# Performance work log

Hardware: AMD Instinct MI355X
Metric: run time of the kernel (lower is better)

## Reference

```python
import jax, jax.numpy as jnp
import numpy as np

B, H_, W_ = 8, 64, 64
N = H_ * W_
IN_DIM = 256
DIM = 256
HEADS = 8
DIM_HEAD = DIM // HEADS      # 32
DH2 = DIM_HEAD // 2          # 16
KC = 3                       # kernel_conv
WS = 8                       # window size
EPS = 1e-5


def _conv2d(x, w, b, groups):
    # x: [B, C, H, W], w: [O, C//groups, kh, kw], 'same' padding, stride 1
    y = jax.lax.conv_general_dilated(
        x, w, window_strides=(1, 1), padding=((1, 1), (1, 1)),
        dimension_numbers=('NCHW', 'OIHW', 'NCHW'), feature_group_count=groups)
    return y + b[None, :, None, None]


def _cross_shaped_attention(q, k, v, H, W, ws, horizontal,
                            fc_w, dep_w, dep_b, rate1, rate2):
    # q, k, v: [B, N, C] with C = dim/2 = 128; H*W == N (no padding path)
    Bq, Nq, C = q.shape
    nh = C // DIM_HEAD  # heads per half = 4
    # ---- parallel conv-attention branch ----
    # [B, 3*heads, dim_head//2, N]
    f = jnp.concatenate([t.reshape(Bq, HEADS, DH2, Nq) for t in (q, k, v)], axis=1)
    # 1x1 conv fc: (heads*3=24) -> (kc*kc=9) channels
    f_all = jnp.einsum('oc,bcst->bost', fc_w, f)           # [B, 9, 16, N]
    f_conv = jnp.transpose(f_all, (0, 2, 1, 3)).reshape(Bq, DH2 * KC * KC, H, W)  # [B,144,H,W]
    out_conv = _conv2d(f_conv, dep_w, dep_b, groups=DH2)   # [B, 128, H, W]
    out_conv = jnp.transpose(out_conv, (0, 2, 3, 1)).reshape(Bq, Nq, C)
    # ---- cross-shaped windowed attention ----
    scale = DIM_HEAD ** -0.5
    if horizontal:
        # window over rows: groups of ws full-width rows -> tokens ws*W
        def win(t):
            t = t.reshape(Bq, H // ws, ws, W, nh, DIM_HEAD)
            return jnp.transpose(t, (0, 1, 4, 2, 3, 5)).reshape(Bq, H // ws, nh, ws * W, DIM_HEAD)
    else:
        # window over cols: groups of ws full-height cols -> tokens ws*H
        def win(t):
            t = t.reshape(Bq, H, W // ws, ws, nh, DIM_HEAD)
            return jnp.transpose(t, (0, 2, 4, 3, 1, 5)).reshape(Bq, W // ws, nh, ws * H, DIM_HEAD)
    qw, kw, vw = win(q), win(k), win(v)
    attn = jnp.einsum('bgnqd,bgnkd->bgnqk', qw, kw) * scale  # [B, G, nh, L, L]
    attn = jax.nn.softmax(attn, axis=-1)
    o = jnp.einsum('bgnqk,bgnkd->bgnqd', attn, vw)           # [B, G, nh, L, dh]
    if horizontal:
        o = o.reshape(Bq, H // ws, nh, ws, W, DIM_HEAD)
        o = jnp.transpose(o, (0, 1, 3, 4, 2, 5)).reshape(Bq, Nq, C)  # B (Hg ws) W (nh dh)
    else:
        o = o.reshape(Bq, W // ws, nh, ws, H, DIM_HEAD)
        o = jnp.transpose(o, (0, 4, 1, 3, 2, 5)).reshape(Bq, Nq, C)  # B H (Wg ws) (nh dh)
    return rate1 * o + rate2 * out_conv


def reference(x, w_qkv, b_qkv, w_out, b_out, bn_g, bn_b, pconv_w, pconv_b,
              fc_w, dep_w, dep_b, rate1, rate2, H, W):
    Bx = x.shape[0]
    Nx = H * W
    qv = x @ w_qkv + b_qkv                       # [B, N, 2*dim]
    q, v = jnp.split(qv, 2, axis=-1)
    # parallel depthwise conv branch on v (hardswish -> dw 3x3)
    v_img = jnp.transpose(v.reshape(Bx, H, W, DIM), (0, 3, 1, 2))
    v_conv = _conv2d(jax.nn.hard_swish(v_img), pconv_w, pconv_b, groups=DIM)
    v_conv = jnp.transpose(v_conv.reshape(Bx, DIM, Nx), (0, 2, 1))   # [B, N, dim]
    qh, qv2 = jnp.split(q, 2, axis=-1)
    vh, vv = jnp.split(v, 2, axis=-1)
    # H % ws == 0 and W % ws == 0 -> no padding, no masks
    attn_h = _cross_shaped_attention(qh, vh, vh, H, W, WS, True,
                                     fc_w, dep_w, dep_b, rate1, rate2)
    attn_v = _cross_shaped_attention(qv2, vv, vv, H, W, WS, False,
                                     fc_w, dep_w, dep_b, rate1, rate2)
    a = jnp.concatenate([attn_h, attn_v], axis=-1) + v_conv
    a = jax.nn.hard_swish(a)
    a = a @ w_out + b_out
    # BatchNorm1d in training mode over flattened (B*N, dim), biased variance
    flat = a.reshape(Bx * Nx, DIM)
    mu = flat.mean(axis=0)
    var = flat.var(axis=0)
    flat = (flat - mu) * jax.lax.rsqrt(var + EPS) * bn_g + bn_b
    return flat.reshape(Bx, Nx, DIM)


def setup_inputs() -> dict:
    key = jax.random.key(0)
    ks = jax.random.split(key, 16)
    s = 0.02
    return {
        'x': jax.random.normal(ks[0], (B, N, IN_DIM), jnp.float32),
        'w_qkv': jax.random.normal(ks[1], (IN_DIM, 2 * DIM), jnp.float32) * s,
        'b_qkv': jax.random.normal(ks[2], (2 * DIM,), jnp.float32) * s,
        'w_out': jax.random.normal(ks[3], (DIM, DIM), jnp.float32) * s,
        'b_out': jax.random.normal(ks[4], (DIM,), jnp.float32) * s,
        'bn_g': jax.random.uniform(ks[5], (DIM,), jnp.float32, 0.5, 1.5),
        'bn_b': jax.random.normal(ks[6], (DIM,), jnp.float32) * s,
        'pconv_w': jax.random.normal(ks[7], (DIM, 1, 3, 3), jnp.float32) * s,
        'pconv_b': jax.random.normal(ks[8], (DIM,), jnp.float32) * s,
        'fc_w': jax.random.normal(ks[9], (KC * KC, HEADS * 3), jnp.float32) * s,
        'dep_w': jax.random.normal(ks[10], (IN_DIM // 2, KC * KC, 3, 3), jnp.float32) * s,
        'dep_b': jax.random.normal(ks[11], (IN_DIM // 2,), jnp.float32) * s,
        'rate1': jax.random.uniform(ks[12], (), jnp.float32, 0.4, 0.6),
        'rate2': jax.random.uniform(ks[13], (), jnp.float32, 0.4, 0.6),
        'H': H_,
        'W': W_,
    }
```

## Files before the change

kernel.cpp:

```cpp
#include <hip/hip_runtime.h>
#include <hip/hip_bf16.h>
#include <math.h>

constexpr int Bn   = 8;
constexpr int Hh   = 64;
constexpr int Ww   = 64;
constexpr int Nn   = Hh * Ww;
constexpr int Mrows = Bn * Nn;
constexpr int QKVC = 512;
constexpr int DIMc = 256;

typedef short short8 __attribute__((ext_vector_type(8)));
typedef float f32x16 __attribute__((ext_vector_type(16)));
typedef float f32x4 __attribute__((ext_vector_type(4)));

__device__ __forceinline__ float hswish(float x) {
    float r = fminf(fmaxf(x + 3.f, 0.f), 6.f);
    return x * r * (1.f / 6.f);
}

__device__ __forceinline__ ushort bf16u(float f) {
    return __bfloat16_as_ushort(__float2bfloat16(f));
}

__device__ __forceinline__ uint32_t pkbf(float a, float b) {
    return (uint32_t)bf16u(a) | ((uint32_t)bf16u(b) << 16);
}

__device__ __forceinline__ float dot2bf(uint32_t a, uint32_t b, float c) {
    asm("v_dot2_f32_bf16 %0, %1, %2, %0" : "+v"(c) : "v"(a), "v"(b));
    return c;
}

__device__ __forceinline__ float bflo(uint32_t p) {
    union { uint32_t u; float f; } c; c.u = p << 16; return c.f;
}
__device__ __forceinline__ float bfhi(uint32_t p) {
    union { uint32_t u; float f; } c; c.u = p & 0xFFFF0000u; return c.f;
}

#if __has_builtin(__builtin_amdgcn_permlane32_swap)
typedef int int2v __attribute__((ext_vector_type(2)));
__device__ __forceinline__ void plswap(uint32_t& a, uint32_t& b) {
    int2v r = __builtin_amdgcn_permlane32_swap((int)a, (int)b, false, false);
    a = (uint32_t)r.x; b = (uint32_t)r.y;
}
#else
__device__ __forceinline__ void plswap(uint32_t& a, uint32_t& b) {
    int l = threadIdx.x & 63;
    uint32_t sa = (uint32_t)__shfl_xor((int)a, 32);
    uint32_t sb = (uint32_t)__shfl_xor((int)b, 32);
    uint32_t na = (l < 32) ? a : sb;
    uint32_t nb = (l < 32) ? sa : b;
    a = na; b = nb;
}
#endif

__device__ __forceinline__ void gload_lds16(const ushort* g, ushort* l) {
    __builtin_amdgcn_global_load_lds(
        (const __attribute__((address_space(1))) unsigned int*)g,
        (__attribute__((address_space(3))) unsigned int*)l, 16, 0, 0);
}

__global__ __launch_bounds__(256) void cvtbf_kernel(
    const float* __restrict__ in, ushort* __restrict__ out)
{
    int i = (blockIdx.x * 256 + threadIdx.x) * 8;
    float4 f0 = *reinterpret_cast<const float4*>(&in[i]);
    float4 f1 = *reinterpret_cast<const float4*>(&in[i + 4]);
    float v[8] = {f0.x, f0.y, f0.z, f0.w, f1.x, f1.y, f1.z, f1.w};
    ushort o[8];
    #pragma unroll
    for (int j = 0; j < 8; ++j) o[j] = bf16u(v[j]);
    *reinterpret_cast<short8*>(&out[i]) = *reinterpret_cast<short8*>(o);
}

__global__ __launch_bounds__(256) void wtconv_kernel(
    const float* __restrict__ Wf, ushort* __restrict__ Wt, int K, int N)
{
    int idx = blockIdx.x * 256 + threadIdx.x;
    int n = idx / K, k = idx - n * K;
    Wt[idx] = bf16u(Wf[(size_t)k * N + n]);
}

__global__ __launch_bounds__(256) void weff_kernel(
    const float* __restrict__ dw, const float* __restrict__ fcw,
    uint32_t* __restrict__ Wp)
{
    int idx = blockIdx.x * 256 + threadIdx.x;
    if (idx >= 9216) return;
    int k = idx % 9;
    int a = (idx / 9) & 7;
    int oc = (idx / 72) & 7;
    int gi = idx / 576;
    float q = 0.f, v = 0.f;
    const float* dwp = &dw[(gi * 8 + oc) * 81 + k];
    #pragma unroll
    for (int ic = 0; ic < 9; ++ic) {
        float d = dwp[ic * 9];
        q += d * fcw[ic * 24 + a];
        v += d * (fcw[ic * 24 + 8 + a] + fcw[ic * 24 + 16 + a]);
    }
    Wp[idx] = pkbf(q, v);
}

template<bool OBF, bool STATS>
__global__ __launch_bounds__(256) void hgemm_kernel(
    const ushort* __restrict__ A, const ushort* __restrict__ Bt,
    const float* __restrict__ bias, void* __restrict__ Cv,
    float* __restrict__ stats, int M, int N, int K)
{
    __shared__ ushort As[128 * 32];
    __shared__ ushort Bs[128 * 32];
    const int tid = threadIdx.x;
    const int w = tid >> 6, l = tid & 63;
    const int brow = blockIdx.y * 128;
    const int bcol = blockIdx.x * 128;
    const int wm = (w >> 1) * 64, wn = (w & 1) * 64;

    f32x4 acc[4][4] = {};

    const int c0 = tid, c1 = tid + 256;
    const int r0 = c0 >> 2, q0 = (c0 & 3) ^ (r0 & 3);
    const int r1 = c1 >> 2, q1 = (c1 & 3) ^ (r1 & 3);
    const ushort* a0p = &A[(size_t)(brow + r0) * K + q0 * 8];
    const ushort* a1p = &A[(size_t)(brow + r1) * K + q1 * 8];
    const ushort* b0p = &Bt[(size_t)(bcol + r0) * K + q0 * 8];
    const ushort* b1p = &Bt[(size_t)(bcol + r1) * K + q1 * 8];
    ushort* asw0 = &As[(w * 64) * 8];
    ushort* asw1 = &As[(256 + w * 64) * 8];
    ushort* bsw0 = &Bs[(w * 64) * 8];
    ushort* bsw1 = &Bs[(256 + w * 64) * 8];

    const int fr = l & 15;
    const int qq = ((l >> 4) ^ (l & 3)) * 8;

    for (int k0 = 0; k0 < K; k0 += 32) {
        gload_lds16(a0p + k0, asw0);
        gload_lds16(a1p + k0, asw1);
        gload_lds16(b0p + k0, bsw0);
        gload_lds16(b1p + k0, bsw1);
        __syncthreads();
        short8 af[4], bf[4];
        #pragma unroll
        for (int i = 0; i < 4; ++i) {
            af[i] = *reinterpret_cast<const short8*>(&As[(wm + i * 16 + fr) * 32 + qq]);
            bf[i] = *reinterpret_cast<const short8*>(&Bs[(wn + i * 16 + fr) * 32 + qq]);
        }
        #pragma unroll
        for (int mi = 0; mi < 4; ++mi)
            #pragma unroll
            for (int ni = 0; ni < 4; ++ni)
                acc[mi][ni] = __builtin_amdgcn_mfma_f32_16x16x32_bf16(
                    af[mi], bf[ni], acc[mi][ni], 0, 0, 0);
        __syncthreads();
    }

    const int cr = l >> 4;
    #pragma unroll
    for (int ni = 0; ni < 4; ++ni) {
        int n = bcol + wn + ni * 16 + fr;
        float bv = bias[n];
        float s1 = 0.f, s2 = 0.f;
        #pragma unroll
        for (int mi = 0; mi < 4; ++mi) {
            int m = brow + wm + mi * 16 + cr * 4;
            #pragma unroll
            for (int r = 0; r < 4; ++r) {
                float val = acc[mi][ni][r] + bv;
                if (OBF)
                    ((ushort*)Cv)[(size_t)(m + r) * N + n] = bf16u(val);
                else
                    ((float*)Cv)[(size_t)(m + r) * N + n] = val;
                if (STATS) { s1 += val; s2 += val * val; }
            }
        }
        if (STATS) {
            s1 += __shfl_xor(s1, 16); s2 += __shfl_xor(s2, 16);
            s1 += __shfl_xor(s1, 32); s2 += __shfl_xor(s2, 32);
            if (cr == 0) {
                atomicAdd(&stats[n], s1);
                atomicAdd(&stats[256 + n], s2);
            }
        }
    }
}

__global__ __launch_bounds__(256) void vconv_kernel(
    const ushort* __restrict__ qvb, const float* __restrict__ pw,
    const float* __restrict__ pb, float* __restrict__ Abuf)
{
    int idx = blockIdx.x * 256 + threadIdx.x;
    int c2 = idx & 127;
    int n = (idx >> 7) & (Nn - 1);
    int b = idx >> 19;
    int x = n & 63, y = n >> 6;
    int ch = c2 * 2;
    float s0 = pb[ch], s1 = pb[ch + 1];
    float w0[9], w1[9];
    #pragma unroll
    for (int k = 0; k < 9; ++k) { w0[k] = pw[ch * 9 + k]; w1[k] = pw[ch * 9 + 9 + k]; }
    #pragma unroll
    for (int ky = 0; ky < 3; ++ky) {
        int yy = y + ky - 1;
        if (yy >= 0 && yy < Hh) {
            #pragma unroll
            for (int kx = 0; kx < 3; ++kx) {
                int xx = x + kx - 1;
                if (xx >= 0 && xx < Ww) {
                    uint32_t pk = *reinterpret_cast<const uint32_t*>(
                        &qvb[(size_t)(b * Nn + yy * Ww + xx) * QKVC + 256 + ch]);
                    s0 += hswish(bflo(pk)) * w0[ky * 3 + kx];
                    s1 += hswish(bfhi(pk)) * w1[ky * 3 + kx];
                }
            }
        }
    }
    float2 o; o.x = s0; o.y = s1;
    *reinterpret_cast<float2*>(&Abuf[(size_t)(b * Nn + n) * DIMc + ch]) = o;
}

__global__ __launch_bounds__(256) void convbranch_kernel(
    const ushort* __restrict__ qvb, const uint32_t* __restrict__ Wp,
    const float* __restrict__ db, const float* __restrict__ rate2p,
    float* __restrict__ Abuf)
{
    int blk = blockIdx.x;
    int ytile = blk & 3;
    int gi = (blk >> 2) & 15;
    int b = (blk >> 6) & 7;
    int branch = blk >> 9;
    int y0 = ytile * 16;
    int qoff = branch * 128;
    int coff = branch * 128;

    __shared__ uint32_t sqv[8][18][66];
    __shared__ uint32_t wpk[8][8][9];
    const int tid = threadIdx.x;

    for (int i = tid; i < 8 * 18 * 66; i += 256) {
        int xp = i % 66;
        int t2 = i / 66;
        int rr = t2 % 18;
        int a = t2 / 18;
        int x = xp - 1;
        int y = y0 + rr - 1;
        uint32_t pk = 0;
        if ((unsigned)x < 64u && (unsigned)y < 64u) {
            int token = (a * 16 + gi) * 32 + (y >> 1);
            int chan = (y & 1) * 64 + x;
            const ushort* p = &qvb[(size_t)(b * Nn + token) * QKVC + qoff + chan];
            pk = (uint32_t)p[0] | ((uint32_t)p[256] << 16);
        }
        sqv[a][rr][xp] = pk;
    }
    for (int i = tid; i < 576; i += 256)
        ((uint32_t*)wpk)[i] = Wp[gi * 576 + i];
    __syncthreads();

    const int x = tid & 63;
    const int w = tid >> 6;
    const int rh = (w & 1) * 8;
    const int oc0 = (w >> 1) * 4;

    float acc[4][8] = {};
    #pragma unroll 1
    for (int a = 0; a < 8; ++a) {
        uint32_t ipk[10][3];
        #pragma unroll
        for (int rr = 0; rr < 10; ++rr) {
            const uint32_t* rp = &sqv[a][rh + rr][x];
            ipk[rr][0] = rp[0]; ipk[rr][1] = rp[1]; ipk[rr][2] = rp[2];
        }
        #pragma unroll
        for (int ocl = 0; ocl < 4; ++ocl) {
            #pragma unroll
            for (int ky = 0; ky < 3; ++ky)
                #pragma unroll
                for (int kx = 0; kx < 3; ++kx) {
                    uint32_t wv = wpk[oc0 + ocl][a][ky * 3 + kx];
                    #pragma unroll
                    for (int row = 0; row < 8; ++row)
                        acc[ocl][row] = dot2bf(ipk[row + ky][kx], wv, acc[ocl][row]);
                }
        }
    }

    __syncthreads();
    float* so = (float*)sqv;
    const float r2 = rate2p[0];
    float dbv[4];
    #pragma unroll
    for (int j = 0; j < 4; ++j) dbv[j] = db[gi * 8 + oc0 + j];
    #pragma unroll
    for (int row = 0; row < 8; ++row) {
        int px = (rh + row) * 64 + x;
        #pragma unroll
        for (int j = 0; j < 4; ++j)
            so[px * 9 + oc0 + j] = r2 * (acc[j][row] + dbv[j]);
    }
    __syncthreads();
    for (int i = tid; i < 8192; i += 256) {
        int px = i >> 3, sl = i & 7;
        int n = (y0 + (px >> 6)) * 64 + (px & 63);
        Abuf[(size_t)(b * Nn + n) * DIMc + coff + gi * 8 + sl] += so[px * 9 + sl];
    }
}

__global__ __launch_bounds__(512) void attn_mfma_kernel(
    const ushort* __restrict__ qvb, const float* __restrict__ rate1p,
    const float* __restrict__ Abuf, ushort* __restrict__ Hb)
{
    int bid = blockIdx.x;
    bool hor = bid < 256;
    int lb = bid & 255;
    int hd = lb & 3;
    int g = (lb >> 2) & 7;
    int b = lb >> 5;
    int half = hor ? 0 : 128;
    int qoff = half + hd * 32;
    int kvoff = 256 + qoff;

    __shared__ __align__(16) char smem[65536];
    char* ldsK  = smem;
    char* ldsVT = smem + 32768;

    const int tid = threadIdx.x;
    const float QS = 0.17677669529663687f * 1.44269504088896f;

    {
        int l = tid;
        int n = hor ? (g * 512 + l) : ((l & 63) * 64 + g * 8 + (l >> 6));
        const ushort* kp = &qvb[(size_t)(b * Nn + n) * QKVC + kvoff];
        uint4 wv[4];
        #pragma unroll
        for (int j = 0; j < 4; ++j)
            wv[j] = *reinterpret_cast<const uint4*>(&kp[j * 8]);
        uint32_t p32[16];
        #pragma unroll
        for (int j = 0; j < 4; ++j) {
            p32[j * 4 + 0] = wv[j].x; p32[j * 4 + 1] = wv[j].y;
            p32[j * 4 + 2] = wv[j].z; p32[j * 4 + 3] = wv[j].w;
        }
        #pragma unroll
        for (int gi = 0; gi < 4; ++gi) {
            uint4 w;
            w.x = p32[gi * 4 + 0]; w.y = p32[gi * 4 + 1];
            w.z = p32[gi * 4 + 2]; w.w = p32[gi * 4 + 3];
            *reinterpret_cast<uint4*>(ldsK + l * 64 + ((gi ^ (l & 3)) << 4)) = w;
        }
        #pragma unroll
        for (int d = 0; d < 32; ++d) {
            ushort us = (ushort)((p32[d >> 1] >> ((d & 1) * 16)) & 0xffff);
            *reinterpret_cast<ushort*>(ldsVT + d * 1024 + ((l * 2) ^ ((d & 7) << 4))) = us;
        }
    }
    __syncthreads();

    const int w = tid >> 6;
    const int lane = tid & 63;
    const int qcol = lane & 31;
    const int hh = lane >> 5;
    const float r1 = rate1p[0];

    #pragma unroll 1
    for (int qt = 0; qt < 2; ++qt) {
        const int q0 = (w * 2 + qt) * 32;
        const int qrow = q0 + qcol;
        const int nq = hor ? (g * 512 + qrow) : ((qrow & 63) * 64 + g * 8 + (qrow >> 6));

        short8 qb[2];
        #pragma unroll
        for (int t = 0; t < 2; ++t) {
            const ushort* qp = &qvb[(size_t)(b * Nn + nq) * QKVC + qoff + t * 16 + hh * 8];
            qb[t] = *reinterpret_cast<const short8*>(qp);
        }

        f32x16 acc = {0,0,0,0,0,0,0,0,0,0,0,0,0,0,0,0};
        float rs = 0.f;

        for (int s = 0; s < 16; ++s) {
            const int k0 = s * 32;
            const int kr = k0 + qcol;
            const short8 a0 = *reinterpret_cast<const short8*>(
                ldsK + kr * 64 + (((0 + hh) ^ (kr & 3)) << 4));
            const short8 a1 = *reinterpret_cast<const short8*>(
                ldsK + kr * 64 + (((2 + hh) ^ (kr & 3)) << 4));
            f32x16 st = {0,0,0,0,0,0,0,0,0,0,0,0,0,0,0,0};
            st = __builtin_amdgcn_mfma_f32_32x32x16_bf16(a0, qb[0], st, 0, 0, 0);
            st = __builtin_amdgcn_mfma_f32_32x32x16_bf16(a1, qb[1], st, 0, 0, 0);

            float p[16];
            #pragma unroll
            for (int r = 0; r < 16; ++r) p[r] = exp2f(st[r] * QS);
            float s01 = (p[0] + p[1]) + (p[2] + p[3]);
            float s23 = (p[4] + p[5]) + (p[6] + p[7]);
            float s45 = (p[8] + p[9]) + (p[10] + p[11]);
            float s67 = (p[12] + p[13]) + (p[14] + p[15]);
            rs += (s01 + s23) + (s45 + s67);

            uint32_t X[8];
            #pragma unroll
            for (int gg = 0; gg < 4; ++gg) {
                X[2 * gg + 0] = pkbf(p[4 * gg + 0], p[4 * gg + 1]);
                X[2 * gg + 1] = pkbf(p[4 * gg + 2], p[4 * gg + 3]);
            }
            #pragma unroll
            for (int u = 0; u < 2; ++u) {
                uint32_t w0 = X[4 * u + 0], w2 = X[4 * u + 2];
                uint32_t w1 = X[4 * u + 1], w3 = X[4 * u + 3];
                plswap(w0, w2);
                plswap(w1, w3);
                union { uint32_t u4[4]; short8 s; } pf;
                pf.u4[0] = w0; pf.u4[1] = w1; pf.u4[2] = w2; pf.u4[3] = w3;
                const int d = qcol;
                const short8 vf = *reinterpret_cast<const short8*>(
                    ldsVT + d * 1024 + ((k0 * 2 + u * 32 + hh * 16) ^ ((d & 7) << 4)));
                acc = __builtin_amdgcn_mfma_f32_32x32x16_bf16(vf, pf.s, acc, 0, 0, 0);
            }
        }

        float rsf = rs + __shfl_xor(rs, 32);
        float scl = r1 / rsf;
        const float* ap = &Abuf[(size_t)(b * Nn + nq) * DIMc + qoff];
        ushort* hp = &Hb[(size_t)(b * Nn + nq) * DIMc + qoff];
        #pragma unroll
        for (int gg = 0; gg < 4; ++gg) {
            int d0 = 8 * gg + 4 * hh;
            float4 o = *reinterpret_cast<const float4*>(&ap[d0]);
            float v0 = hswish(o.x + acc[4 * gg + 0] * scl);
            float v1 = hswish(o.y + acc[4 * gg + 1] * scl);
            float v2 = hswish(o.z + acc[4 * gg + 2] * scl);
            float v3 = hswish(o.w + acc[4 * gg + 3] * scl);
            uint2 pk; pk.x = pkbf(v0, v1); pk.y = pkbf(v2, v3);
            *reinterpret_cast<uint2*>(&hp[d0]) = pk;
        }
    }
}

__global__ __launch_bounds__(256) void bnnorm_kernel(
    const float* __restrict__ Y, const float* __restrict__ stats,
    const float* __restrict__ g, const float* __restrict__ bta,
    float* __restrict__ out)
{
    int idx = blockIdx.x * 256 + threadIdx.x;
    int c = idx & 255;
    float mu = stats[c] * (1.f / (float)Mrows);
    float var = stats[256 + c] * (1.f / (float)Mrows) - mu * mu;
    float inv = rsqrtf(var + 1e-5f);
    out[idx] = (Y[idx] - mu) * inv * g[c] + bta[c];
}

extern "C" void kernel_launch(void* const* d_in, const int* in_sizes, int n_in,
                              void* d_out, int out_size, void* d_ws, size_t ws_size,
                              hipStream_t stream)
{
    const float* x      = (const float*)d_in[0];
    const float* w_qkv  = (const float*)d_in[1];
    const float* b_qkv  = (const float*)d_in[2];
    const float* w_out  = (const float*)d_in[3];
    const float* b_out  = (const float*)d_in[4];
    const float* bn_g   = (const float*)d_in[5];
    const float* bn_b   = (const float*)d_in[6];
    const float* pconv_w = (const float*)d_in[7];
    const float* pconv_b = (const float*)d_in[8];
    const float* fc_w   = (const float*)d_in[9];
    const float* dep_w  = (const float*)d_in[10];
    const float* dep_b  = (const float*)d_in[11];
    const float* rate1  = (const float*)d_in[12];
    const float* rate2  = (const float*)d_in[13];
    float* out = (float*)d_out;

    char* ws = (char*)d_ws;
    ushort* qvb   = (ushort*)(ws);
    ushort* Hb    = (ushort*)(ws + (32u << 20));
    ushort* xb    = (ushort*)(ws + (64u << 20));
    float*  Abuf  = (float*)(ws + (64u << 20));
    float*  Ybuf  = (float*)(ws + (96u << 20));
    float*  stats = (float*)(ws + (128u << 20));
    ushort* Wt1   = (ushort*)(ws + (128u << 20) + 4096);
    ushort* Wt2   = (ushort*)(ws + (128u << 20) + 4096 + (256u << 10));
    uint32_t* Wp  = (uint32_t*)(ws + (128u << 20) + 4096 + (384u << 10));

    wtconv_kernel<<<(512 * 256) / 256, 256, 0, stream>>>(w_qkv, Wt1, 256, 512);
    wtconv_kernel<<<(256 * 256) / 256, 256, 0, stream>>>(w_out, Wt2, 256, 256);
    weff_kernel<<<36, 256, 0, stream>>>(dep_w, fc_w, Wp);
    cvtbf_kernel<<<(Mrows * 256 / 8) / 256, 256, 0, stream>>>(x, xb);

    hgemm_kernel<true, false><<<dim3(4, 256), 256, 0, stream>>>(
        xb, Wt1, b_qkv, qvb, nullptr, Mrows, 512, 256);

    vconv_kernel<<<(Mrows * 128) / 256, 256, 0, stream>>>(qvb, pconv_w, pconv_b, Abuf);

    convbranch_kernel<<<1024, 256, 0, stream>>>(qvb, Wp, dep_b, rate2, Abuf);

    attn_mfma_kernel<<<512, 512, 0, stream>>>(qvb, rate1, Abuf, Hb);

    hipMemsetAsync(stats, 0, 2 * 256 * sizeof(float), stream);
    hgemm_kernel<false, true><<<dim3(2, 256), 256, 0, stream>>>(
        Hb, Wt2, b_out, Ybuf, stats, Mrows, 256, 256);

    bnnorm_kernel<<<(Mrows * 256) / 256, 256, 0, stream>>>(Ybuf, stats, bn_g, bn_b, out);
}
```

Baseline: 231.5 us.

## Store conv-branch accumulator in bf16, reorder conv kernels, vectorize BN

The intermediate Abuf that combines the positional conv and conv-attention branch is now held in bf16 instead of fp32, which halves its traffic. The conv branch now runs first and writes directly from registers with 8-row tiles and coalesced paired loads. The vconv kernel then read-modify-writes its sum, and the shared-memory staging plus the read-modify-write in convbranch are gone. The BN normalize kernel is vectorized to float4. The cost is extra bf16 rounding in the summed branch outputs, which could affect accuracy.

```diff
diff --git a/kernel.cpp b/kernel.cpp
--- a/kernel.cpp
+++ b/kernel.cpp
@@ -188,7 +188,7 @@
 
 __global__ __launch_bounds__(256) void vconv_kernel(
     const ushort* __restrict__ qvb, const float* __restrict__ pw,
-    const float* __restrict__ pb, float* __restrict__ Abuf)
+    const float* __restrict__ pb, ushort* __restrict__ Abuf)
 {
     int idx = blockIdx.x * 256 + threadIdx.x;
     int c2 = idx & 127;
@@ -216,43 +216,56 @@
             }
         }
     }
-    float2 o; o.x = s0; o.y = s1;
-    *reinterpret_cast<float2*>(&Abuf[(size_t)(b * Nn + n) * DIMc + ch]) = o;
+    uint32_t* ap = reinterpret_cast<uint32_t*>(&Abuf[(size_t)(b * Nn + n) * DIMc + ch]);
+    uint32_t cur = *ap;
+    *ap = pkbf(bflo(cur) + s0, bfhi(cur) + s1);
 }
 
 __global__ __launch_bounds__(256) void convbranch_kernel(
     const ushort* __restrict__ qvb, const uint32_t* __restrict__ Wp,
     const float* __restrict__ db, const float* __restrict__ rate2p,
-    float* __restrict__ Abuf)
+    ushort* __restrict__ Abuf)
 {
     int blk = blockIdx.x;
-    int ytile = blk & 3;
-    int gi = (blk >> 2) & 15;
-    int b = (blk >> 6) & 7;
-    int branch = blk >> 9;
-    int y0 = ytile * 16;
+    int ytile = blk & 7;
+    int gi = (blk >> 3) & 15;
+    int b = (blk >> 7) & 7;
+    int branch = blk >> 10;
+    int y0 = ytile * 8;
     int qoff = branch * 128;
     int coff = branch * 128;
 
-    __shared__ uint32_t sqv[8][18][66];
+    __shared__ uint32_t sqv[8][10][68];
     __shared__ uint32_t wpk[8][8][9];
     const int tid = threadIdx.x;
 
-    for (int i = tid; i < 8 * 18 * 66; i += 256) {
-        int xp = i % 66;
-        int t2 = i / 66;
-        int rr = t2 % 18;
-        int a = t2 / 18;
-        int x = xp - 1;
-        int y = y0 + rr - 1;
-        uint32_t pk = 0;
-        if ((unsigned)x < 64u && (unsigned)y < 64u) {
-            int token = (a * 16 + gi) * 32 + (y >> 1);
-            int chan = (y & 1) * 64 + x;
-            const ushort* p = &qvb[(size_t)(b * Nn + token) * QKVC + qoff + chan];
-            pk = (uint32_t)p[0] | ((uint32_t)p[256] << 16);
-        }
-        sqv[a][rr][xp] = pk;
+    if (tid < 160) {
+        int r = tid >> 1;
+        int col = 1 + (tid & 1) * 65;
+        sqv[r / 10][r % 10][col] = 0;
+    }
+    {
+        const int x2 = (tid & 31) * 2;
+        int rr = tid >> 5;
+        int a = 0;
+        const size_t bbase = (size_t)(b * Nn) * QKVC + qoff;
+        #pragma unroll
+        for (int it = 0; it < 10; ++it) {
+            int y = y0 + rr - 1;
+            uint32_t lo = 0, hi = 0;
+            if ((unsigned)y < 64u) {
+                int token = (a * 16 + gi) * 32 + (y >> 1);
+                size_t base = bbase + (size_t)token * QKVC + (y & 1) * 64 + x2;
+                uint32_t q = *reinterpret_cast<const uint32_t*>(&qvb[base]);
+                uint32_t v = *reinterpret_cast<const uint32_t*>(&qvb[base + 256]);
+                lo = (q & 0xffffu) | (v << 16);
+                hi = (q >> 16) | (v & 0xffff0000u);
+            }
+            uint2 wv; wv.x = lo; wv.y = hi;
+            *reinterpret_cast<uint2*>(&sqv[a][rr][2 + x2]) = wv;
+            rr += 8;
+            if (rr >= 10) { rr -= 10; a += 1; }
+        }
     }
     for (int i = tid; i < 576; i += 256)
         ((uint32_t*)wpk)[i] = Wp[gi * 576 + i];
@@ -260,17 +273,17 @@
 
     const int x = tid & 63;
     const int w = tid >> 6;
-    const int rh = (w & 1) * 8;
+    const int rh = (w & 1) * 4;
     const int oc0 = (w >> 1) * 4;
 
-    float acc[4][8] = {};
+    float acc[4][4] = {};
     #pragma unroll 1
     for (int a = 0; a < 8; ++a) {
-        uint32_t ipk[10][3];
-        #pragma unroll
-        for (int rr = 0; rr < 10; ++rr) {
-            const uint32_t* rp = &sqv[a][rh + rr][x];
-            ipk[rr][0] = rp[0]; ipk[rr][1] = rp[1]; ipk[rr][2] = rp[2];
+        uint32_t ipk[6][3];
+        #pragma unroll
+        for (int j = 0; j < 6; ++j) {
+            const uint32_t* rp = &sqv[a][rh + j][1 + x];
+            ipk[j][0] = rp[0]; ipk[j][1] = rp[1]; ipk[j][2] = rp[2];
         }
         #pragma unroll
         for (int ocl = 0; ocl < 4; ++ocl) {
@@ -280,36 +293,30 @@
                 for (int kx = 0; kx < 3; ++kx) {
                     uint32_t wv = wpk[oc0 + ocl][a][ky * 3 + kx];
                     #pragma unroll
-                    for (int row = 0; row < 8; ++row)
-                        acc[ocl][row] = dot2bf(ipk[row + ky][kx], wv, acc[ocl][row]);
+                    for (int ro = 0; ro < 4; ++ro)
+                        acc[ocl][ro] = dot2bf(ipk[ro + ky][kx], wv, acc[ocl][ro]);
                 }
         }
     }
 
-    __syncthreads();
-    float* so = (float*)sqv;
     const float r2 = rate2p[0];
     float dbv[4];
     #pragma unroll
     for (int j = 0; j < 4; ++j) dbv[j] = db[gi * 8 + oc0 + j];
     #pragma unroll
-    for (int row = 0; row < 8; ++row) {
-        int px = (rh + row) * 64 + x;
-        #pragma unroll
-        for (int j = 0; j < 4; ++j)
-            so[px * 9 + oc0 + j] = r2 * (acc[j][row] + dbv[j]);
-    }
-    __syncthreads();
-    for (int i = tid; i < 8192; i += 256) {
-        int px = i >> 3, sl = i & 7;
-        int n = (y0 + (px >> 6)) * 64 + (px & 63);
-        Abuf[(size_t)(b * Nn + n) * DIMc + coff + gi * 8 + sl] += so[px * 9 + sl];
+    for (int ro = 0; ro < 4; ++ro) {
+        int n = (y0 + rh + ro) * 64 + x;
+        uint2 pk;
+        pk.x = pkbf(r2 * (acc[0][ro] + dbv[0]), r2 * (acc[1][ro] + dbv[1]));
+        pk.y = pkbf(r2 * (acc[2][ro] + dbv[2]), r2 * (acc[3][ro] + dbv[3]));
+        *reinterpret_cast<uint2*>(
+            &Abuf[(size_t)(b * Nn + n) * DIMc + coff + gi * 8 + oc0]) = pk;
     }
 }
 
 __global__ __launch_bounds__(512) void attn_mfma_kernel(
     const ushort* __restrict__ qvb, const float* __restrict__ rate1p,
-    const float* __restrict__ Abuf, ushort* __restrict__ Hb)
+    const ushort* __restrict__ Abuf, ushort* __restrict__ Hb)
 {
     int bid = blockIdx.x;
     bool hor = bid < 256;
@@ -422,16 +429,16 @@
 
         float rsf = rs + __shfl_xor(rs, 32);
         float scl = r1 / rsf;
-        const float* ap = &Abuf[(size_t)(b * Nn + nq) * DIMc + qoff];
+        const ushort* ap = &Abuf[(size_t)(b * Nn + nq) * DIMc + qoff];
         ushort* hp = &Hb[(size_t)(b * Nn + nq) * DIMc + qoff];
         #pragma unroll
         for (int gg = 0; gg < 4; ++gg) {
             int d0 = 8 * gg + 4 * hh;
-            float4 o = *reinterpret_cast<const float4*>(&ap[d0]);
-            float v0 = hswish(o.x + acc[4 * gg + 0] * scl);
-            float v1 = hswish(o.y + acc[4 * gg + 1] * scl);
-            float v2 = hswish(o.z + acc[4 * gg + 2] * scl);
-            float v3 = hswish(o.w + acc[4 * gg + 3] * scl);
+            uint2 av = *reinterpret_cast<const uint2*>(&ap[d0]);
+            float v0 = hswish(bflo(av.x) + acc[4 * gg + 0] * scl);
+            float v1 = hswish(bfhi(av.x) + acc[4 * gg + 1] * scl);
+            float v2 = hswish(bflo(av.y) + acc[4 * gg + 2] * scl);
+            float v3 = hswish(bfhi(av.y) + acc[4 * gg + 3] * scl);
             uint2 pk; pk.x = pkbf(v0, v1); pk.y = pkbf(v2, v3);
             *reinterpret_cast<uint2*>(&hp[d0]) = pk;
         }
@@ -443,12 +450,26 @@
     const float* __restrict__ g, const float* __restrict__ bta,
     float* __restrict__ out)
 {
-    int idx = blockIdx.x * 256 + threadIdx.x;
-    int c = idx & 255;
-    float mu = stats[c] * (1.f / (float)Mrows);
-    float var = stats[256 + c] * (1.f / (float)Mrows) - mu * mu;
-    float inv = rsqrtf(var + 1e-5f);
-    out[idx] = (Y[idx] - mu) * inv * g[c] + bta[c];
+    int i4 = (blockIdx.x * 256 + threadIdx.x) * 4;
+    int c = i4 & 255;
+    float4 y = *reinterpret_cast<const float4*>(&Y[i4]);
+    float4 mu = *reinterpret_cast<const float4*>(&stats[c]);
+    float4 s2 = *reinterpret_cast<const float4*>(&stats[256 + c]);
+    float4 gg = *reinterpret_cast<const float4*>(&g[c]);
+    float4 bb = *reinterpret_cast<const float4*>(&bta[c]);
+    const float inv_m = 1.f / (float)Mrows;
+    float4 o;
+    {
+        float m = mu.x * inv_m, v = s2.x * inv_m - m * m;
+        o.x = (y.x - m) * rsqrtf(v + 1e-5f) * gg.x + bb.x;
+        m = mu.y * inv_m; v = s2.y * inv_m - m * m;
+        o.y = (y.y - m) * rsqrtf(v + 1e-5f) * gg.y + bb.y;
+        m = mu.z * inv_m; v = s2.z * inv_m - m * m;
+        o.z = (y.z - m) * rsqrtf(v + 1e-5f) * gg.z + bb.z;
+        m = mu.w * inv_m; v = s2.w * inv_m - m * m;
+        o.w = (y.w - m) * rsqrtf(v + 1e-5f) * gg.w + bb.w;
+    }
+    *reinterpret_cast<float4*>(&out[i4]) = o;
 }
 
 extern "C" void kernel_launch(void* const* d_in, const int* in_sizes, int n_in,
@@ -474,8 +495,8 @@
     char* ws = (char*)d_ws;
     ushort* qvb   = (ushort*)(ws);
     ushort* Hb    = (ushort*)(ws + (32u << 20));
+    ushort* Abuf  = (ushort*)(ws + (48u << 20));
     ushort* xb    = (ushort*)(ws + (64u << 20));
-    float*  Abuf  = (float*)(ws + (64u << 20));
     float*  Ybuf  = (float*)(ws + (96u << 20));
     float*  stats = (float*)(ws + (128u << 20));
     ushort* Wt1   = (ushort*)(ws + (128u << 20) + 4096);
@@ -490,9 +511,9 @@
     hgemm_kernel<true, false><<<dim3(4, 256), 256, 0, stream>>>(
         xb, Wt1, b_qkv, qvb, nullptr, Mrows, 512, 256);
 
+    convbranch_kernel<<<2048, 256, 0, stream>>>(qvb, Wp, dep_b, rate2, Abuf);
+
     vconv_kernel<<<(Mrows * 128) / 256, 256, 0, stream>>>(qvb, pconv_w, pconv_b, Abuf);
-
-    convbranch_kernel<<<1024, 256, 0, stream>>>(qvb, Wp, dep_b, rate2, Abuf);
 
     attn_mfma_kernel<<<512, 512, 0, stream>>>(qvb, rate1, Abuf, Hb);
 
@@ -500,5 +521,5 @@
     hgemm_kernel<false, true><<<dim3(2, 256), 256, 0, stream>>>(
         Hb, Wt2, b_out, Ybuf, stats, Mrows, 256, 256);
 
-    bnnorm_kernel<<<(Mrows * 256) / 256, 256, 0, stream>>>(Ybuf, stats, bn_g, bn_b, out);
-}
+    bnnorm_kernel<<<(Mrows * 256 / 4) / 256, 256, 0, stream>>>(Ybuf, stats, bn_g, bn_b, out);
+}
```

Result: faster. 200.9 us (-13.2%).
